# Optimization experiments

Hardware: AMD Instinct MI355X
Metric: run time of the kernel (lower is better)

The kernel has to match this reference:

```python
import jax, jax.numpy as jnp
import numpy as np

ALPHA = 1.0

def _soft_assign(x, clusters, alpha=ALPHA):
    # (avoids materializing the (N, K, D) broadcast intermediate)
    x_sq = jnp.sum(x * x, axis=1, keepdims=True)            # (N, 1)
    c_sq = jnp.sum(clusters * clusters, axis=1)             # (K,)
    cross = jnp.einsum('nd,kd->nk', x, clusters)            # (N, K)
    dist_sq = jnp.maximum(x_sq + c_sq[None, :] - 2.0 * cross, 0.0)
    q = 1.0 / (1.0 + dist_sq / alpha)
    q = q ** ((alpha + 1.0) / 2.0)
    return q / jnp.sum(q, axis=1, keepdims=True)            # row-normalize

def setup_inputs() -> dict:
    key = jax.random.key(0)
    k1, k2 = jax.random.split(key)
    N, D, K = 65536, 512, 1024
    x = jax.random.normal(k1, (N, D), dtype=jnp.float32)
    # xavier_uniform for (K, D): limit = sqrt(6 / (K + D))
    limit = float(np.sqrt(6.0 / (K + D)))
    clusters = jax.random.uniform(k2, (K, D), dtype=jnp.float32, minval=-limit, maxval=limit)
    return {"x": x, "clusters": clusters}

def reference(x, clusters):
    return _soft_assign(x, clusters)
```

## Files before the change

kernel.cpp:

```cpp
#include <hip/hip_runtime.h>

typedef __bf16 bf16x8 __attribute__((ext_vector_type(8)));
typedef float f32x16 __attribute__((ext_vector_type(16)));
typedef unsigned short ushort8 __attribute__((ext_vector_type(8)));

__device__ __forceinline__ unsigned short f2bf(float f) {
    unsigned int u = __float_as_uint(f);
    u += 0x7FFFu + ((u >> 16) & 1u);
    return (unsigned short)(u >> 16);
}

__global__ __launch_bounds__(256) void prep_clusters(
    const float* __restrict__ cl, unsigned short* __restrict__ cbf,
    float* __restrict__ csq) {
    const int row  = blockIdx.x * 4 + (threadIdx.x >> 6);
    const int lane = threadIdx.x & 63;
    const float4* cg = (const float4*)(cl + ((size_t)row << 9) + lane * 8);
    float4 v0 = cg[0], v1 = cg[1];
    float ssq = v0.x*v0.x + v0.y*v0.y + v0.z*v0.z + v0.w*v0.w
              + v1.x*v1.x + v1.y*v1.y + v1.z*v1.z + v1.w*v1.w;
    ushort8 h;
    h[0]=f2bf(v0.x); h[1]=f2bf(v0.y); h[2]=f2bf(v0.z); h[3]=f2bf(v0.w);
    h[4]=f2bf(v1.x); h[5]=f2bf(v1.y); h[6]=f2bf(v1.z); h[7]=f2bf(v1.w);
    const int n = row & 31, T = row >> 5;
    const int s = lane >> 1, hh = lane & 1;
    *(ushort8*)(cbf + (size_t)((T * 32 + s) * 64 + hh * 32 + n) * 8) = h;
#pragma unroll
    for (int off = 32; off >= 1; off >>= 1) ssq += __shfl_xor(ssq, off);
    if (lane == 0) csq[row] = ssq;
}

__global__ __launch_bounds__(1024, 4) void soft_assign(
    const float* __restrict__ x, const unsigned short* __restrict__ cbf,
    const float* __restrict__ csq, float* __restrict__ out) {
    __shared__ unsigned short xs[2048 * 8];
    __shared__ float part[64 * 32];
    __shared__ float xsq[64];
    __shared__ float inv[64];

    const int t    = threadIdx.x;
    const int lane = t & 63;
    const int w    = t >> 6;
    const int l31  = lane & 31;
    const int half = lane >> 5;
    const int rb   = blockIdx.x;

    part[t] = 0.f;
    part[t + 1024] = 0.f;
    if (t < 64) xsq[t] = 0.f;

    const int col0   = w * 64 + l31;
    const float csq0 = csq[col0];
    const float csq1 = csq[col0 + 32];

    f32x16 c00, c01, c10, c11;
#pragma unroll
    for (int i = 0; i < 16; ++i) { c00[i] = 0.f; c01[i] = 0.f; c10[i] = 0.f; c11[i] = 0.f; }

    const unsigned short* bT0 = cbf + ((size_t)(2 * w) * 32 * 64 + lane) * 8;
    const unsigned short* bT1 = cbf + ((size_t)(2 * w + 1) * 32 * 64 + lane) * 8;
    const unsigned short* aB  = xs + lane * 8;

    bf16x8 b0c = *(const bf16x8*)(bT0);
    bf16x8 b1c = *(const bf16x8*)(bT1);
    bf16x8 b0n = *(const bf16x8*)(bT0 + 512);
    bf16x8 b1n = *(const bf16x8*)(bT1 + 512);

#pragma unroll 1
    for (int ch = 0; ch < 2; ++ch) {
        if (ch) __syncthreads();
#pragma unroll
        for (int i = 0; i < 2; ++i) {
            const int g  = 2 * t + i;
            const int l  = g & 63;
            const int sl = (g >> 6) & 15;
            const int mt = g >> 10;
            const int row = mt * 32 + (l & 31);
            const int d0  = ch * 256 + sl * 16 + (l >> 5) * 8;
            const float4* xg = (const float4*)(x + (size_t)(rb * 64 + row) * 512 + d0);
            float4 v0 = xg[0], v1 = xg[1];
            ushort8 h;
            h[0]=f2bf(v0.x); h[1]=f2bf(v0.y); h[2]=f2bf(v0.z); h[3]=f2bf(v0.w);
            h[4]=f2bf(v1.x); h[5]=f2bf(v1.y); h[6]=f2bf(v1.z); h[7]=f2bf(v1.w);
            *(ushort8*)(xs + (size_t)g * 8) = h;
            float ss = v0.x*v0.x + v0.y*v0.y + v0.z*v0.z + v0.w*v0.w
                     + v1.x*v1.x + v1.y*v1.y + v1.z*v1.z + v1.w*v1.w;
            atomicAdd(&xsq[row], ss);
        }
        __syncthreads();

#pragma unroll 1
        for (int sl = 0; sl < 16; sl += 2) {
            const int sg  = ch * 16 + sl;
            const int sp2 = (sg + 2) & 31;
            const int sp3 = (sg + 3) & 31;
            bf16x8 p0 = *(const bf16x8*)(bT0 + sp2 * 512);
            bf16x8 p1 = *(const bf16x8*)(bT1 + sp2 * 512);
            bf16x8 q0 = *(const bf16x8*)(bT0 + sp3 * 512);
            bf16x8 q1 = *(const bf16x8*)(bT1 + sp3 * 512);
            bf16x8 a0 = *(const bf16x8*)(aB + (sl)     * 512);
            bf16x8 a1 = *(const bf16x8*)(aB + 8192 + (sl)     * 512);
            bf16x8 a2 = *(const bf16x8*)(aB + (sl + 1) * 512);
            bf16x8 a3 = *(const bf16x8*)(aB + 8192 + (sl + 1) * 512);
            c00 = __builtin_amdgcn_mfma_f32_32x32x16_bf16(a0, b0c, c00, 0, 0, 0);
            c01 = __builtin_amdgcn_mfma_f32_32x32x16_bf16(a0, b1c, c01, 0, 0, 0);
            c10 = __builtin_amdgcn_mfma_f32_32x32x16_bf16(a1, b0c, c10, 0, 0, 0);
            c11 = __builtin_amdgcn_mfma_f32_32x32x16_bf16(a1, b1c, c11, 0, 0, 0);
            c00 = __builtin_amdgcn_mfma_f32_32x32x16_bf16(a2, b0n, c00, 0, 0, 0);
            c01 = __builtin_amdgcn_mfma_f32_32x32x16_bf16(a2, b1n, c01, 0, 0, 0);
            c10 = __builtin_amdgcn_mfma_f32_32x32x16_bf16(a3, b0n, c10, 0, 0, 0);
            c11 = __builtin_amdgcn_mfma_f32_32x32x16_bf16(a3, b1n, c11, 0, 0, 0);
            b0c = p0; b1c = p1; b0n = q0; b1n = q1;
        }
    }

#pragma unroll
    for (int r = 0; r < 16; ++r) {
        const int rl0 = (r & 3) + 8 * (r >> 2) + 4 * half;
        const float x0 = xsq[rl0];
        const float x1 = xsq[rl0 + 32];
        float q00 = __builtin_amdgcn_rcpf(1.f + fmaxf(x0 + csq0 - 2.f * c00[r], 0.f));
        float q01 = __builtin_amdgcn_rcpf(1.f + fmaxf(x0 + csq1 - 2.f * c01[r], 0.f));
        float q10 = __builtin_amdgcn_rcpf(1.f + fmaxf(x1 + csq0 - 2.f * c10[r], 0.f));
        float q11 = __builtin_amdgcn_rcpf(1.f + fmaxf(x1 + csq1 - 2.f * c11[r], 0.f));
        c00[r] = q00; c01[r] = q01; c10[r] = q10; c11[r] = q11;
        atomicAdd(&part[rl0 * 32 + l31], q00 + q01);
        atomicAdd(&part[(rl0 + 32) * 32 + l31], q10 + q11);
    }
    __syncthreads();
    if (t < 64) {
        float s = 0.f;
#pragma unroll
        for (int c = 0; c < 32; ++c) s += part[t * 32 + ((c + t) & 31)];
        inv[t] = __builtin_amdgcn_rcpf(s);
    }
    __syncthreads();

    float* og = out + (size_t)rb * 64 * 1024;
#pragma unroll
    for (int r = 0; r < 16; ++r) {
        const int rl0 = (r & 3) + 8 * (r >> 2) + 4 * half;
        const float i0 = inv[rl0];
        const float i1 = inv[rl0 + 32];
        og[(size_t)rl0 * 1024 + col0]             = c00[r] * i0;
        og[(size_t)rl0 * 1024 + col0 + 32]        = c01[r] * i0;
        og[(size_t)(rl0 + 32) * 1024 + col0]      = c10[r] * i1;
        og[(size_t)(rl0 + 32) * 1024 + col0 + 32] = c11[r] * i1;
    }
}

extern "C" void kernel_launch(void* const* d_in, const int* in_sizes, int n_in,
                              void* d_out, int out_size, void* d_ws, size_t ws_size,
                              hipStream_t stream) {
    const float* x  = (const float*)d_in[0];
    const float* cl = (const float*)d_in[1];
    float* out = (float*)d_out;

    unsigned short* cbf = (unsigned short*)d_ws;
    float* csq = (float*)((char*)d_ws + (size_t)1024 * 512 * 2);

    prep_clusters<<<256, 256, 0, stream>>>(cl, cbf, csq);
    soft_assign<<<1024, 1024, 0, stream>>>(x, cbf, csq, out);
}
```

Measured before the change: 569.5 us.

## Pre-convert x to bf16 and run a persistent double-buffered kernel with async LDS loads

```diff
diff --git a/kernel.cpp b/kernel.cpp
--- a/kernel.cpp
+++ b/kernel.cpp
@@ -9,6 +9,190 @@
     u += 0x7FFFu + ((u >> 16) & 1u);
     return (unsigned short)(u >> 16);
 }
+
+
+__global__ __launch_bounds__(256) void prep_all(
+    const float* __restrict__ x, const float* __restrict__ cl,
+    unsigned short* __restrict__ xbf, unsigned short* __restrict__ cbf,
+    float* __restrict__ csq, float* __restrict__ xsq) {
+    const int bid = blockIdx.x;
+    const int t   = threadIdx.x;
+    if (bid < 4096) {
+        const int gx  = bid * 256 + t;
+        const int row = gx >> 4, c = gx & 15;
+        const float4* xg = (const float4*)(x + ((size_t)row << 9) + c * 32);
+        float4 v[8];
+#pragma unroll
+        for (int i = 0; i < 8; ++i) v[i] = xg[i];
+        float ssq = 0.f;
+#pragma unroll
+        for (int i = 0; i < 8; ++i)
+            ssq += v[i].x*v[i].x + v[i].y*v[i].y + v[i].z*v[i].z + v[i].w*v[i].w;
+#pragma unroll
+        for (int off = 1; off <= 8; off <<= 1) ssq += __shfl_xor(ssq, off);
+        if ((t & 15) == 0) xsq[row] = ssq;
+
+        const int rb = row >> 6, mt = (row >> 5) & 1, n = row & 31;
+#pragma unroll
+        for (int g = 0; g < 4; ++g) {
+            const float4 a = v[2*g], b = v[2*g+1];
+            ushort8 h;
+            h[0]=f2bf(a.x); h[1]=f2bf(a.y); h[2]=f2bf(a.z); h[3]=f2bf(a.w);
+            h[4]=f2bf(b.x); h[5]=f2bf(b.y); h[6]=f2bf(b.z); h[7]=f2bf(b.w);
+            const int d0 = c * 32 + g * 8;
+            const int sl = d0 >> 4, kh = (d0 >> 3) & 1;
+            *(ushort8*)(xbf + (size_t)rb * 32768 +
+                        (size_t)(((mt * 32 + sl) * 64 + kh * 32 + n)) * 8) = h;
+        }
+    } else {
+        const int row  = (bid - 4096) * 4 + (t >> 6);
+        const int lane = t & 63;
+        const float4* cg = (const float4*)(cl + ((size_t)row << 9) + lane * 8);
+        float4 v0 = cg[0], v1 = cg[1];
+        float ssq = v0.x*v0.x + v0.y*v0.y + v0.z*v0.z + v0.w*v0.w
+                  + v1.x*v1.x + v1.y*v1.y + v1.z*v1.z + v1.w*v1.w;
+        ushort8 h;
+        h[0]=f2bf(v0.x); h[1]=f2bf(v0.y); h[2]=f2bf(v0.z); h[3]=f2bf(v0.w);
+        h[4]=f2bf(v1.x); h[5]=f2bf(v1.y); h[6]=f2bf(v1.z); h[7]=f2bf(v1.w);
+        const int n = row & 31, T = row >> 5;
+        const int s = lane >> 1, hh = lane & 1;
+        *(ushort8*)(cbf + (size_t)((T * 32 + s) * 64 + hh * 32 + n) * 8) = h;
+#pragma unroll
+        for (int off = 32; off >= 1; off >>= 1) ssq += __shfl_xor(ssq, off);
+        if (lane == 0) csq[row] = ssq;
+    }
+}
+
+__device__ __forceinline__ void stage_a(const unsigned short* __restrict__ src,
+                                        unsigned short* dst) {
+#pragma unroll
+    for (int i = 0; i < 4; ++i)
+        __builtin_amdgcn_global_load_lds(
+            (const __attribute__((address_space(1))) unsigned int*)(src + i * 512),
+            (__attribute__((address_space(3))) unsigned int*)(dst + i * 512),
+            16, 0, 0);
+}
+
+__global__ __launch_bounds__(1024, 4) void soft_assign2(
+    const unsigned short* __restrict__ xbf, const unsigned short* __restrict__ cbf,
+    const float* __restrict__ csq, const float* __restrict__ xsq,
+    float* __restrict__ out) {
+    __shared__ unsigned short xs[2][32768];
+    __shared__ float part[64 * 32];
+    __shared__ float xsql[2][64];
+    __shared__ float inv[64];
+
+    const int t    = threadIdx.x;
+    const int lane = t & 63;
+    const int w    = t >> 6;
+    const int l31  = lane & 31;
+    const int half = lane >> 5;
+
+    part[t] = 0.f;
+    part[t + 1024] = 0.f;
+
+    const int col0   = w * 64 + l31;
+    const float csq0 = csq[col0];
+    const float csq1 = csq[col0 + 32];
+
+    const unsigned short* bT0 = cbf + ((size_t)(2 * w) * 2048 + lane) * 8;
+    const unsigned short* bT1 = bT0 + 16384;
+
+    stage_a(xbf + (size_t)blockIdx.x * 32768 + (w * 4) * 512 + lane * 8,
+            &xs[0][(w * 4) * 512]);
+    if (t < 64) xsql[0][t] = xsq[blockIdx.x * 64 + t];
+    asm volatile("s_waitcnt vmcnt(0)" ::: "memory");
+    __syncthreads();
+
+    int buf = 0;
+#pragma unroll 1
+    for (int ri = 0; ri < 4; ++ri) {
+        const int rb = blockIdx.x + 256 * ri;
+        const unsigned short* aB = &xs[buf][0] + lane * 8;
+
+        f32x16 c00, c01, c10, c11;
+#pragma unroll
+        for (int i = 0; i < 16; ++i) { c00[i]=0.f; c01[i]=0.f; c10[i]=0.f; c11[i]=0.f; }
+
+        bf16x8 b0c = *(const bf16x8*)(bT0);
+        bf16x8 b1c = *(const bf16x8*)(bT1);
+        bf16x8 b0n = *(const bf16x8*)(bT0 + 512);
+        bf16x8 b1n = *(const bf16x8*)(bT1 + 512);
+
+#pragma unroll 4
+        for (int sl = 0; sl < 32; sl += 2) {
+            const int sp2 = (sl + 2) & 31;
+            const int sp3 = (sl + 3) & 31;
+            bf16x8 p0 = *(const bf16x8*)(bT0 + sp2 * 512);
+            bf16x8 p1 = *(const bf16x8*)(bT1 + sp2 * 512);
+            bf16x8 q0 = *(const bf16x8*)(bT0 + sp3 * 512);
+            bf16x8 q1 = *(const bf16x8*)(bT1 + sp3 * 512);
+            bf16x8 a0 = *(const bf16x8*)(aB + sl * 512);
+            bf16x8 a1 = *(const bf16x8*)(aB + 16384 + sl * 512);
+            bf16x8 a2 = *(const bf16x8*)(aB + (sl + 1) * 512);
+            bf16x8 a3 = *(const bf16x8*)(aB + 16384 + (sl + 1) * 512);
+            __builtin_amdgcn_s_setprio(1);
+            c00 = __builtin_amdgcn_mfma_f32_32x32x16_bf16(a0, b0c, c00, 0, 0, 0);
+            c01 = __builtin_amdgcn_mfma_f32_32x32x16_bf16(a0, b1c, c01, 0, 0, 0);
+            c10 = __builtin_amdgcn_mfma_f32_32x32x16_bf16(a1, b0c, c10, 0, 0, 0);
+            c11 = __builtin_amdgcn_mfma_f32_32x32x16_bf16(a1, b1c, c11, 0, 0, 0);
+            c00 = __builtin_amdgcn_mfma_f32_32x32x16_bf16(a2, b0n, c00, 0, 0, 0);
+            c01 = __builtin_amdgcn_mfma_f32_32x32x16_bf16(a2, b1n, c01, 0, 0, 0);
+            c10 = __builtin_amdgcn_mfma_f32_32x32x16_bf16(a3, b0n, c10, 0, 0, 0);
+            c11 = __builtin_amdgcn_mfma_f32_32x32x16_bf16(a3, b1n, c11, 0, 0, 0);
+            __builtin_amdgcn_s_setprio(0);
+            b0c = p0; b1c = p1; b0n = q0; b1n = q1;
+        }
+
+        if (ri < 3) {
+            stage_a(xbf + (size_t)(rb + 256) * 32768 + (w * 4) * 512 + lane * 8,
+                    &xs[buf ^ 1][(w * 4) * 512]);
+            if (t < 64) xsql[buf ^ 1][t] = xsq[(rb + 256) * 64 + t];
+        }
+
+        const float* xq = xsql[buf];
+#pragma unroll
+        for (int r = 0; r < 16; ++r) {
+            const int rl0 = (r & 3) + 8 * (r >> 2) + 4 * half;
+            const float x0 = xq[rl0];
+            const float x1 = xq[rl0 + 32];
+            float q00 = __builtin_amdgcn_rcpf(1.f + fmaxf(x0 + csq0 - 2.f * c00[r], 0.f));
+            float q01 = __builtin_amdgcn_rcpf(1.f + fmaxf(x0 + csq1 - 2.f * c01[r], 0.f));
+            float q10 = __builtin_amdgcn_rcpf(1.f + fmaxf(x1 + csq0 - 2.f * c10[r], 0.f));
+            float q11 = __builtin_amdgcn_rcpf(1.f + fmaxf(x1 + csq1 - 2.f * c11[r], 0.f));
+            c00[r] = q00; c01[r] = q01; c10[r] = q10; c11[r] = q11;
+            atomicAdd(&part[rl0 * 32 + l31], q00 + q01);
+            atomicAdd(&part[(rl0 + 32) * 32 + l31], q10 + q11);
+        }
+        __syncthreads();
+        if (t < 64) {
+            float s = 0.f;
+#pragma unroll
+            for (int c2 = 0; c2 < 32; ++c2) {
+                const int idx = t * 32 + ((c2 + t) & 31);
+                s += part[idx];
+                part[idx] = 0.f;
+            }
+            inv[t] = __builtin_amdgcn_rcpf(s);
+        }
+        asm volatile("s_waitcnt vmcnt(0)" ::: "memory");
+        __syncthreads();
+
+        float* og = out + (size_t)rb * 65536;
+#pragma unroll
+        for (int r = 0; r < 16; ++r) {
+            const int rl0 = (r & 3) + 8 * (r >> 2) + 4 * half;
+            const float i0 = inv[rl0];
+            const float i1 = inv[rl0 + 32];
+            og[(size_t)rl0 * 1024 + col0]             = c00[r] * i0;
+            og[(size_t)rl0 * 1024 + col0 + 32]        = c01[r] * i0;
+            og[(size_t)(rl0 + 32) * 1024 + col0]      = c10[r] * i1;
+            og[(size_t)(rl0 + 32) * 1024 + col0 + 32] = c11[r] * i1;
+        }
+        buf ^= 1;
+    }
+}
+
 
 __global__ __launch_bounds__(256) void prep_clusters(
     const float* __restrict__ cl, unsigned short* __restrict__ cbf,
@@ -156,9 +340,23 @@
     const float* cl = (const float*)d_in[1];
     float* out = (float*)d_out;
 
-    unsigned short* cbf = (unsigned short*)d_ws;
-    float* csq = (float*)((char*)d_ws + (size_t)1024 * 512 * 2);
-
-    prep_clusters<<<256, 256, 0, stream>>>(cl, cbf, csq);
-    soft_assign<<<1024, 1024, 0, stream>>>(x, cbf, csq, out);
-}
+    const size_t CBF_OFF = 0;
+    const size_t CSQ_OFF = 1048576;
+    const size_t XSQ_OFF = 1052672;
+    const size_t XBF_OFF = 1314816;
+    const size_t NEED    = 68423680;
+
+    if (ws_size >= NEED) {
+        unsigned short* cbf = (unsigned short*)((char*)d_ws + CBF_OFF);
+        float*          csq = (float*)((char*)d_ws + CSQ_OFF);
+        float*          xsq = (float*)((char*)d_ws + XSQ_OFF);
+        unsigned short* xbf = (unsigned short*)((char*)d_ws + XBF_OFF);
+        prep_all<<<4352, 256, 0, stream>>>(x, cl, xbf, cbf, csq, xsq);
+        soft_assign2<<<256, 1024, 0, stream>>>(xbf, cbf, csq, xsq, out);
+    } else {
+        unsigned short* cbf = (unsigned short*)d_ws;
+        float* csq = (float*)((char*)d_ws + (size_t)1024 * 512 * 2);
+        prep_clusters<<<256, 256, 0, stream>>>(cl, cbf, csq);
+        soft_assign<<<1024, 1024, 0, stream>>>(x, cbf, csq, out);
+    }
+}
```

Result: slower. 645.7 us, median of 2 (+13.4%).
